# Kernel tuning notes

Measured on AMD Instinct MI355X. Metric: run time of the kernel, lower is better.

The kernel has to match this reference:

```python
import jax, jax.numpy as jnp
import numpy as np

N_POINTS = 16384
N_SAMPLES = 8192


def setup_inputs() -> dict:
    key = jax.random.key(0)
    k1, k2, k3, k4 = jax.random.split(key, 4)
    a = jax.random.normal(k1, (3, N_POINTS), dtype=jnp.float32)
    b = jax.random.normal(k2, (3, N_POINTS), dtype=jnp.float32)
    # stand-ins for np.random.shuffle(...)[:n_samples] in the torch forward
    a_idx = jax.random.randint(k3, (N_SAMPLES,), 0, N_POINTS, dtype=jnp.int64)
    b_idx = jax.random.randint(k4, (N_SAMPLES,), 0, N_POINTS, dtype=jnp.int64)
    return {"a": a, "b": b, "a_idx": a_idx, "b_idx": b_idx}


def reference(a, b, a_idx, b_idx):
    # a, b: [3, N]; sample n_samples columns, transpose -> [n, 3], keep xyz
    pa = a[:, a_idx].T[:, :3]  # [n, 3]
    pb = b[:, b_idx].T[:, :3]  # [n, 3]
    # d[k, i] = ||pa_i - pb_k||^2, via ||a||^2 + ||b||^2 - 2 b.a^T
    # (avoids the original's [n, n, 3] broadcasted difference tensor)
    sq_a = jnp.sum(pa * pa, axis=1)  # [n]
    sq_b = jnp.sum(pb * pb, axis=1)  # [n]
    d = sq_a[None, :] + sq_b[:, None] - 2.0 * (pb @ pa.T)  # [n, n]
    # torch.min(d, 0)[0].sum(): min over b-points for each a-point, then sum
    return jnp.min(d, axis=0).sum()
```

## Files before the change

### kernel.cpp

```cpp
#include <hip/hip_runtime.h>
#include <stdint.h>


#define BLOCK   256
#define NPTS_A  4
#define BPTS    64

__device__ __forceinline__ unsigned enc_f32(float f) {
    unsigned u = __float_as_uint(f);
    return (u & 0x80000000u) ? ~u : (u | 0x80000000u);
}
__device__ __forceinline__ float dec_f32(unsigned u) {
    return (u & 0x80000000u) ? __uint_as_float(u & 0x7FFFFFFFu)
                             : __uint_as_float(~u);
}

__global__ __launch_bounds__(128)
void chamfer_pack_kernel(const float* __restrict__ a,
                         const float* __restrict__ b,
                         const int* __restrict__ a_idx,
                         const int* __restrict__ b_idx,
                         float4* __restrict__ pa4,
                         float4* __restrict__ pb4,
                         unsigned* __restrict__ minarr,
                         float* __restrict__ out,
                         int N, int n) {
    int i = blockIdx.x * 128 + threadIdx.x;
    if (i < n) {
        int ai = a_idx[i];
        float x = a[ai], y = a[N + ai], z = a[2 * N + ai];
        pa4[i] = make_float4(x, y, z, x * x + y * y + z * z);
        int bi = b_idx[i];
        float u = b[bi], v = b[N + bi], w = b[2 * N + bi];
        pb4[i] = make_float4(-2.f * u, -2.f * v, -2.f * w,
                             u * u + v * v + w * w);
        minarr[i] = 0xFFFFFFFFu;
    }
    if (i == 0) out[0] = 0.f;
}

__global__ __launch_bounds__(BLOCK)
void chamfer_min_kernel(const float4* __restrict__ pa4,
                        const float4* __restrict__ pb4,
                        unsigned* __restrict__ minarr,
                        int a_chunks) {
    __shared__ float4 tile[BPTS];
    const int bid = blockIdx.x;
    const int ac  = bid % a_chunks;
    const int bc  = bid / a_chunks;
    const int tid = threadIdx.x;
    const int APB = BLOCK * NPTS_A;

    if (tid < BPTS)
        tile[tid] = pb4[bc * BPTS + tid];
    __syncthreads();

    float ax[NPTS_A], ay[NPTS_A], az[NPTS_A], mn[NPTS_A];
#pragma unroll
    for (int m = 0; m < NPTS_A; ++m) {
        float4 p = pa4[ac * APB + m * BLOCK + tid];
        ax[m] = p.x; ay[m] = p.y; az[m] = p.z;
        mn[m] = 3.4e38f;
    }

#pragma unroll 8
    for (int k = 0; k < BPTS; ++k) {
        float4 t = tile[k];
#pragma unroll
        for (int m = 0; m < NPTS_A; ++m) {
            float c = fmaf(t.x, ax[m], fmaf(t.y, ay[m], fmaf(t.z, az[m], t.w)));
            mn[m] = fminf(mn[m], c);
        }
    }

#pragma unroll
    for (int m = 0; m < NPTS_A; ++m)
        atomicMin(&minarr[ac * APB + m * BLOCK + tid], enc_f32(mn[m]));
}

__global__ __launch_bounds__(BLOCK)
void chamfer_reduce_kernel(const float4* __restrict__ pa4,
                           const unsigned* __restrict__ minarr,
                           float* __restrict__ out) {
    __shared__ float wsum[BLOCK / 64];
    const int tid = threadIdx.x;
    const int i = blockIdx.x * BLOCK + tid;

    float v = dec_f32(minarr[i]) + pa4[i].w;

#pragma unroll
    for (int off = 32; off > 0; off >>= 1)
        v += __shfl_down(v, off, 64);
    if ((tid & 63) == 0) wsum[tid >> 6] = v;
    __syncthreads();
    if (tid == 0) {
        float s = 0.f;
#pragma unroll
        for (int w = 0; w < BLOCK / 64; ++w) s += wsum[w];
        atomicAdd(out, s);
    }
}

extern "C" void kernel_launch(void* const* d_in, const int* in_sizes, int n_in,
                              void* d_out, int out_size, void* d_ws, size_t ws_size,
                              hipStream_t stream) {
    const float* a     = (const float*)d_in[0];
    const float* b     = (const float*)d_in[1];
    const int*   a_idx = (const int*)d_in[2];
    const int*   b_idx = (const int*)d_in[3];
    float*       out   = (float*)d_out;

    const int N = in_sizes[0] / 3;
    const int n = in_sizes[2];

    const int a_chunks = n / (BLOCK * NPTS_A);

    float4*   pa4    = (float4*)d_ws;
    float4*   pb4    = pa4 + n;
    unsigned* minarr = (unsigned*)(pb4 + n);

    chamfer_pack_kernel<<<n / 128, 128, 0, stream>>>(
        a, b, a_idx, b_idx, pa4, pb4, minarr, out, N, n);

    chamfer_min_kernel<<<a_chunks * (n / BPTS), BLOCK, 0, stream>>>(
        pa4, pb4, minarr, a_chunks);

    chamfer_reduce_kernel<<<n / BLOCK, BLOCK, 0, stream>>>(
        pa4, minarr, out);
}
```

Baseline: 69.38 us.

## Fuse min and sum into one kernel with double-buffered LDS b-chunks

Restructures the chamfer kernel so each block owns 16 a-points and scans all b-points in 1024-point chunks staged through double-buffered, padded shared memory with register prefetch. The per-point minimum is reduced with wave shuffles and shared memory, and the sum is accumulated directly, removing the atomicMin buffer and the separate reduce launch. The trade-off is fewer, longer-running blocks with lower parallelism per block.

New measurement: 75.78 us. 9.2% more time.

```diff
diff --git a/kernel.cpp b/kernel.cpp
--- a/kernel.cpp
+++ b/kernel.cpp
@@ -2,18 +2,12 @@
 #include <stdint.h>
 
 
-#define BLOCK   256
-#define NPTS_A  4
-#define BPTS    64
-
-__device__ __forceinline__ unsigned enc_f32(float f) {
-    unsigned u = __float_as_uint(f);
-    return (u & 0x80000000u) ? ~u : (u | 0x80000000u);
-}
-__device__ __forceinline__ float dec_f32(unsigned u) {
-    return (u & 0x80000000u) ? __uint_as_float(u & 0x7FFFFFFFu)
-                             : __uint_as_float(~u);
-}
+#define MT    256
+#define APB   16
+#define NPA   4
+#define CH    1024
+#define NCH   8
+#define CPAD  (CH + CH / 16)
 
 __global__ __launch_bounds__(128)
 void chamfer_pack_kernel(const float* __restrict__ a,
@@ -22,7 +16,6 @@
                          const int* __restrict__ b_idx,
                          float4* __restrict__ pa4,
                          float4* __restrict__ pb4,
-                         unsigned* __restrict__ minarr,
                          float* __restrict__ out,
                          int N, int n) {
     int i = blockIdx.x * 128 + threadIdx.x;
@@ -34,70 +27,84 @@
         float u = b[bi], v = b[N + bi], w = b[2 * N + bi];
         pb4[i] = make_float4(-2.f * u, -2.f * v, -2.f * w,
                              u * u + v * v + w * w);
-        minarr[i] = 0xFFFFFFFFu;
     }
     if (i == 0) out[0] = 0.f;
 }
 
-__global__ __launch_bounds__(BLOCK)
+__global__ __launch_bounds__(MT)
 void chamfer_min_kernel(const float4* __restrict__ pa4,
                         const float4* __restrict__ pb4,
-                        unsigned* __restrict__ minarr,
-                        int a_chunks) {
-    __shared__ float4 tile[BPTS];
-    const int bid = blockIdx.x;
-    const int ac  = bid % a_chunks;
-    const int bc  = bid / a_chunks;
-    const int tid = threadIdx.x;
-    const int APB = BLOCK * NPTS_A;
+                        float* __restrict__ out) {
+    __shared__ float4 tile[2][CPAD];
+    __shared__ float  red[4][APB];
 
-    if (tid < BPTS)
-        tile[tid] = pb4[bc * BPTS + tid];
-    __syncthreads();
+    const int t = threadIdx.x;
+    const int g = t & 3;
+    const int s = t >> 2;
+    const int abase = blockIdx.x * APB;
 
-    float ax[NPTS_A], ay[NPTS_A], az[NPTS_A], mn[NPTS_A];
+    float ax[NPA], ay[NPA], az[NPA], mn[NPA];
 #pragma unroll
-    for (int m = 0; m < NPTS_A; ++m) {
-        float4 p = pa4[ac * APB + m * BLOCK + tid];
+    for (int m = 0; m < NPA; ++m) {
+        float4 p = pa4[abase + g * NPA + m];
         ax[m] = p.x; ay[m] = p.y; az[m] = p.z;
         mn[m] = 3.4e38f;
     }
 
-#pragma unroll 8
-    for (int k = 0; k < BPTS; ++k) {
-        float4 t = tile[k];
+    float4 r0 = pb4[t], r1 = pb4[t + 256], r2 = pb4[t + 512], r3 = pb4[t + 768];
+
+    for (int c = 0; c < NCH; ++c) {
+        float4* tl = tile[c & 1];
+        {
+            int u;
+            u = t;        tl[u + (u >> 4)] = r0;
+            u = t + 256;  tl[u + (u >> 4)] = r1;
+            u = t + 512;  tl[u + (u >> 4)] = r2;
+            u = t + 768;  tl[u + (u >> 4)] = r3;
+        }
+        __syncthreads();
+        if (c + 1 < NCH) {
+            const float4* src = pb4 + (c + 1) * CH;
+            r0 = src[t]; r1 = src[t + 256]; r2 = src[t + 512]; r3 = src[t + 768];
+        }
+        const float4* row = &tl[s * 17];
 #pragma unroll
-        for (int m = 0; m < NPTS_A; ++m) {
-            float c = fmaf(t.x, ax[m], fmaf(t.y, ay[m], fmaf(t.z, az[m], t.w)));
-            mn[m] = fminf(mn[m], c);
+        for (int j = 0; j < 16; ++j) {
+            float4 bt = row[j];
+#pragma unroll
+            for (int m = 0; m < NPA; ++m) {
+                float d = fmaf(bt.x, ax[m],
+                          fmaf(bt.y, ay[m],
+                          fmaf(bt.z, az[m], bt.w)));
+                mn[m] = fminf(mn[m], d);
+            }
         }
     }
 
 #pragma unroll
-    for (int m = 0; m < NPTS_A; ++m)
-        atomicMin(&minarr[ac * APB + m * BLOCK + tid], enc_f32(mn[m]));
-}
-
-__global__ __launch_bounds__(BLOCK)
-void chamfer_reduce_kernel(const float4* __restrict__ pa4,
-                           const unsigned* __restrict__ minarr,
-                           float* __restrict__ out) {
-    __shared__ float wsum[BLOCK / 64];
-    const int tid = threadIdx.x;
-    const int i = blockIdx.x * BLOCK + tid;
-
-    float v = dec_f32(minarr[i]) + pa4[i].w;
-
+    for (int m = 0; m < NPA; ++m) {
+        float v = mn[m];
+        v = fminf(v, __shfl_xor(v, 4, 64));
+        v = fminf(v, __shfl_xor(v, 8, 64));
+        v = fminf(v, __shfl_xor(v, 16, 64));
+        v = fminf(v, __shfl_xor(v, 32, 64));
+        mn[m] = v;
+    }
+    if ((t & 63) < 4) {
 #pragma unroll
-    for (int off = 32; off > 0; off >>= 1)
-        v += __shfl_down(v, off, 64);
-    if ((tid & 63) == 0) wsum[tid >> 6] = v;
+        for (int m = 0; m < NPA; ++m)
+            red[t >> 6][(t & 3) * NPA + m] = mn[m];
+    }
     __syncthreads();
-    if (tid == 0) {
-        float s = 0.f;
-#pragma unroll
-        for (int w = 0; w < BLOCK / 64; ++w) s += wsum[w];
-        atomicAdd(out, s);
+    if (t < APB) {
+        float v = fminf(fminf(red[0][t], red[1][t]),
+                        fminf(red[2][t], red[3][t]));
+        v += pa4[abase + t].w;
+        v += __shfl_down(v, 8, 16);
+        v += __shfl_down(v, 4, 16);
+        v += __shfl_down(v, 2, 16);
+        v += __shfl_down(v, 1, 16);
+        if (t == 0) atomicAdd(out, v);
     }
 }
 
@@ -113,18 +120,11 @@
     const int N = in_sizes[0] / 3;
     const int n = in_sizes[2];
 
-    const int a_chunks = n / (BLOCK * NPTS_A);
-
-    float4*   pa4    = (float4*)d_ws;
-    float4*   pb4    = pa4 + n;
-    unsigned* minarr = (unsigned*)(pb4 + n);
+    float4* pa4 = (float4*)d_ws;
+    float4* pb4 = pa4 + n;
 
     chamfer_pack_kernel<<<n / 128, 128, 0, stream>>>(
-        a, b, a_idx, b_idx, pa4, pb4, minarr, out, N, n);
+        a, b, a_idx, b_idx, pa4, pb4, out, N, n);
 
-    chamfer_min_kernel<<<a_chunks * (n / BPTS), BLOCK, 0, stream>>>(
-        pa4, pb4, minarr, a_chunks);
-
-    chamfer_reduce_kernel<<<n / BLOCK, BLOCK, 0, stream>>>(
-        pa4, minarr, out);
+    chamfer_min_kernel<<<n / APB, MT, 0, stream>>>(pa4, pb4, out);
 }
```
